# Kernel optimization log

Measured on AMD Instinct MI355X. Metric: run time of the kernel, lower is better.

Reference implementation:

```python
import jax, jax.numpy as jnp
import numpy as np

B, H, P, L = 8, 512, 512, 2048
HIGH_STAB, LOW_STAB = 0.9, 0.99  # 0 <= high < |lambda| <= low <= 1 (discrete dynamics)


def setup_inputs() -> dict:
    key = jax.random.key(0)
    k_u, k_mag, k_ph, k_b, k_c, k_d = jax.random.split(key, 6)
    u = jax.random.normal(k_u, (B, H, L), dtype=jnp.float32)
    # Frozen diagonal reservoir state matrix Lambda_bar: complex eigenvalues with
    # magnitude in (high_stability, low_stability], random phase (stored as real/imag pairs).
    mag = jax.random.uniform(k_mag, (P,), minval=HIGH_STAB, maxval=LOW_STAB)
    phase = jax.random.uniform(k_ph, (P,), minval=0.0, maxval=2.0 * np.pi)
    Lambda_bar_ri = jnp.stack([mag * jnp.cos(phase), mag * jnp.sin(phase)], axis=-1)  # (P,2)
    B_bar_ri = jax.random.normal(k_b, (P, H, 2), dtype=jnp.float32)  # complex B_bar as real pairs
    C_ri = jax.random.normal(k_c, (H, P, 2), dtype=jnp.float32)      # complex C as real pairs
    D = jax.random.normal(k_d, (H, H), dtype=jnp.float32)
    return {"u": u, "Lambda_bar_ri": Lambda_bar_ri, "B_bar_ri": B_bar_ri, "C_ri": C_ri, "D": D}


def _binary_op(e_i, e_j):
    A_i, Bu_i = e_i
    A_j, Bu_j = e_j
    return (A_j * A_i, A_j * Bu_i + Bu_j)


def reference(u, Lambda_bar_ri, B_bar_ri, C_ri, D):
    Lam = jax.lax.complex(Lambda_bar_ri[:, 0], Lambda_bar_ri[:, 1])        # (P,)
    B_bar = jax.lax.complex(B_bar_ri[..., 0], B_bar_ri[..., 1])            # (P,H)
    C = jax.lax.complex(C_ri[..., 0], C_ri[..., 1])                        # (H,P)
    # Bu_t = B_bar @ u_t for all t, batched: (B,P,L) complex
    Bu = jnp.einsum('ph,bhl->bpl', B_bar, u.astype(B_bar.dtype))
    A = jnp.broadcast_to(Lam[None, :, None], Bu.shape)                     # (B,P,L)
    # Parallel associative scan: x_t = Lam * x_{t-1} + Bu_t
    _, x = jax.lax.associative_scan(_binary_op, (A, Bu), axis=2)           # (B,P,L)
    C_A_Bu = jnp.einsum('hp,bpl->bhl', C, x).real                          # (B,H,L)
    # torch.einsum('hh,bhl->bhl', D, u) uses only the diagonal of D
    Du = jnp.diagonal(D)[None, :, None] * u
    return jax.nn.gelu(C_A_Bu + Du, approximate=False)
```

## Files before the change

kernel.cpp:

```cpp
#include <hip/hip_runtime.h>
#include <cstdint>
#include <cstddef>

#define BB 8
#define HH 512
#define PP 512
#define LL 2048

typedef __attribute__((ext_vector_type(8))) __bf16 bf16x8;
typedef __attribute__((ext_vector_type(4))) float f32x4;

__device__ __forceinline__ uint16_t f2bf(float f) {
  uint32_t u = __builtin_bit_cast(uint32_t, f);
  u += 0x7FFFu + ((u >> 16) & 1u);
  return (uint16_t)(u >> 16);
}

__device__ __forceinline__ void async_copy16(const void* gptr, void* ldsptr) {
  __builtin_amdgcn_global_load_lds(
      (const __attribute__((address_space(1))) unsigned int*)gptr,
      (__attribute__((address_space(3))) unsigned int*)ldsptr,
      16, 0, 0);
}

__global__ __launch_bounds__(256) void prep_and_transpose(
    const float* __restrict__ U, const float* __restrict__ Bbar,
    const float* __restrict__ Cri, const float* __restrict__ Dm,
    uint16_t* __restrict__ Ut, uint16_t* __restrict__ A1,
    uint16_t* __restrict__ A2, float* __restrict__ Dd) {
  __shared__ uint16_t tile[64][66];
  const int t = threadIdx.x;
  if (blockIdx.x < 2048) {
    const int bid = blockIdx.x;
    const int b = bid >> 8;
    const int h0 = ((bid >> 5) & 7) * 64;
    const int l0 = (bid & 31) * 64;
    const int r = t >> 2, c = t & 3;
    const float* src = U + ((size_t)(b * 512 + h0 + r)) * 2048 + l0 + c * 16;
#pragma unroll
    for (int q = 0; q < 4; ++q) {
      float4 v = *(const float4*)(src + q * 4);
      *(uint32_t*)&tile[r][c * 16 + q * 4]     = (uint32_t)f2bf(v.x) | ((uint32_t)f2bf(v.y) << 16);
      *(uint32_t*)&tile[r][c * 16 + q * 4 + 2] = (uint32_t)f2bf(v.z) | ((uint32_t)f2bf(v.w) << 16);
    }
    __syncthreads();
    uint16_t* dst = Ut + ((size_t)(b * 2048 + l0 + r)) * 512 + h0 + c * 16;
    uint32_t o[8];
#pragma unroll
    for (int k = 0; k < 8; ++k)
      o[k] = (uint32_t)tile[c * 16 + 2 * k][r] | ((uint32_t)tile[c * 16 + 2 * k + 1][r] << 16);
    *(uint4*)(dst)     = make_uint4(o[0], o[1], o[2], o[3]);
    *(uint4*)(dst + 8) = make_uint4(o[4], o[5], o[6], o[7]);
  } else {
    int idx = (blockIdx.x - 2048) * 256 + t;
    int p = idx >> 9, h = idx & 511;
    A1[(size_t)p * 512 + h]          = f2bf(Bbar[((size_t)p * 512 + h) * 2 + 0]);
    A1[(size_t)(512 + p) * 512 + h]  = f2bf(Bbar[((size_t)p * 512 + h) * 2 + 1]);
    int h2 = idx >> 9, p2 = idx & 511;
    A2[(size_t)h2 * 1024 + p2]        = f2bf( Cri[((size_t)h2 * 512 + p2) * 2 + 0]);
    A2[(size_t)h2 * 1024 + 512 + p2]  = f2bf(-Cri[((size_t)h2 * 512 + p2) * 2 + 1]);
    if (idx < 512) Dd[idx] = Dm[(size_t)idx * 512 + idx];
  }
}

__global__ __launch_bounds__(512) void scan_tr(
    const float* __restrict__ Lam, const uint16_t* __restrict__ Bu,
    uint16_t* __restrict__ Xt8) {
  __shared__ uint16_t S[16][2048];
  const int t = threadIdx.x, wave = t >> 6, lane = t & 63;
  const int b = blockIdx.x >> 6, p0 = (blockIdx.x & 63) * 8, p = p0 + wave;

  const float lr = Lam[p * 2 + 0], li = Lam[p * 2 + 1];
  float ar = lr, ai = li;
#pragma unroll
  for (int s = 0; s < 5; ++s) { float nr = ar * ar - ai * ai, ni = 2.f * ar * ai; ar = nr; ai = ni; }

  const uint16_t* rowre = Bu + ((size_t)(b * 1024 + p)) * 2048 + lane * 32;
  const uint16_t* rowim = Bu + ((size_t)(b * 1024 + 512 + p)) * 2048 + lane * 32;
  uint4 vr[4], vi[4];
#pragma unroll
  for (int q = 0; q < 4; ++q) { vr[q] = ((const uint4*)rowre)[q]; vi[q] = ((const uint4*)rowim)[q]; }

  float xr[32], xi[32];
  float sr = 0.f, si = 0.f;
#pragma unroll
  for (int q = 0; q < 4; ++q) {
    uint32_t wr[4] = {vr[q].x, vr[q].y, vr[q].z, vr[q].w};
    uint32_t wi[4] = {vi[q].x, vi[q].y, vi[q].z, vi[q].w};
#pragma unroll
    for (int d = 0; d < 4; ++d) {
      float br0 = __builtin_bit_cast(float, wr[d] << 16);
      float bi0 = __builtin_bit_cast(float, wi[d] << 16);
      float br1 = __builtin_bit_cast(float, wr[d] & 0xFFFF0000u);
      float bi1 = __builtin_bit_cast(float, wi[d] & 0xFFFF0000u);
      int j = q * 8 + d * 2;
      float nr = lr * sr - li * si + br0, ni = lr * si + li * sr + bi0;
      sr = nr; si = ni; xr[j] = sr; xi[j] = si;
      nr = lr * sr - li * si + br1; ni = lr * si + li * sr + bi1;
      sr = nr; si = ni; xr[j + 1] = sr; xi[j + 1] = si;
    }
  }
  float Ar = ar, Ai = ai, Sr = sr, Si = si;
#pragma unroll
  for (int off = 1; off < 64; off <<= 1) {
    float pAr = __shfl_up(Ar, off), pAi = __shfl_up(Ai, off);
    float pSr = __shfl_up(Sr, off), pSi = __shfl_up(Si, off);
    if (lane >= off) {
      float tSr = Ar * pSr - Ai * pSi + Sr;
      float tSi = Ar * pSi + Ai * pSr + Si;
      float tAr = Ar * pAr - Ai * pAi;
      float tAi = Ar * pAi + Ai * pAr;
      Sr = tSr; Si = tSi; Ar = tAr; Ai = tAi;
    }
  }
  float Cr = __shfl_up(Sr, 1), Ci = __shfl_up(Si, 1);
  if (lane == 0) { Cr = 0.f; Ci = 0.f; }
  float fr_ = lr * Cr - li * Ci, fi_ = lr * Ci + li * Cr;
#pragma unroll
  for (int j = 0; j < 32; ++j) {
    xr[j] += fr_; xi[j] += fi_;
    float nfr = fr_ * lr - fi_ * li, nfi = fr_ * li + fi_ * lr;
    fr_ = nfr; fi_ = nfi;
  }
#pragma unroll
  for (int q = 0; q < 4; ++q) {
    uint32_t wr[4], wi[4];
#pragma unroll
    for (int d = 0; d < 4; ++d) {
      int j = q * 8 + d * 2;
      wr[d] = (uint32_t)f2bf(xr[j]) | ((uint32_t)f2bf(xr[j + 1]) << 16);
      wi[d] = (uint32_t)f2bf(xi[j]) | ((uint32_t)f2bf(xi[j + 1]) << 16);
    }
    *(uint4*)&S[wave * 2 + 0][lane * 32 + q * 8] = make_uint4(wr[0], wr[1], wr[2], wr[3]);
    *(uint4*)&S[wave * 2 + 1][lane * 32 + q * 8] = make_uint4(wi[0], wi[1], wi[2], wi[3]);
  }
  __syncthreads();
  const size_t gre = (size_t)b * 128 + (p0 >> 3);
#pragma unroll
  for (int c = 0; c < 2; ++c) {
    uint16_t* dst = Xt8 + (gre + (size_t)c * 64) * 2048 * 8;
#pragma unroll
    for (int rep = 0; rep < 4; ++rep) {
      int l = rep * 512 + t;
      uint32_t o0 = (uint32_t)S[0 + c][l] | ((uint32_t)S[2 + c][l] << 16);
      uint32_t o1 = (uint32_t)S[4 + c][l] | ((uint32_t)S[6 + c][l] << 16);
      uint32_t o2 = (uint32_t)S[8 + c][l] | ((uint32_t)S[10 + c][l] << 16);
      uint32_t o3 = (uint32_t)S[12 + c][l] | ((uint32_t)S[14 + c][l] << 16);
      *(uint4*)(dst + (size_t)l * 8) = make_uint4(o0, o1, o2, o3);
    }
  }
}

#define GEMM_CORE(KDIM, PB0_EXPR, BSTRIDE)                                    \
  constexpr int K = (KDIM), NT = K / 32;                                      \
  __shared__ __align__(16) uint16_t Alds[3][128 * 32];                        \
  __shared__ __align__(16) uint16_t Blds[3][64 * 32];                         \
  const int t = threadIdx.x, lane = t & 63, w = t >> 6;                       \
  const int m0 = blockIdx.y * 128, n0 = blockIdx.x * 64, b = blockIdx.z;      \
  const int r0 = t >> 2;                                                      \
  const int c0 = (t & 3) ^ ((r0 >> 1) & 3);                                   \
  const uint16_t* pA0 = Amat + (size_t)(m0 + r0) * K + c0 * 8;                \
  const uint16_t* pA1 = Amat + (size_t)(m0 + 64 + r0) * K + c0 * 8;           \
  const uint16_t* pB0 = (PB0_EXPR);                                           \
  const int d0 = t * 8;                                                       \
  const int wm = (w >> 1) * 64, wn = (w & 1) * 32;                            \
  const int fr = lane & 15, fq = lane >> 4;                                   \
  int offA[4], offB[2];                                                       \
  _Pragma("unroll")                                                           \
  for (int i = 0; i < 4; ++i) {                                               \
    int rm = wm + i * 16 + fr;                                                \
    offA[i] = rm * 32 + ((fq ^ ((rm >> 1) & 3)) * 8);                         \
  }                                                                           \
  _Pragma("unroll")                                                           \
  for (int j = 0; j < 2; ++j) {                                               \
    int rn = wn + j * 16 + fr;                                                \
    offB[j] = rn * 32 + ((fq ^ ((rn >> 1) & 3)) * 8);                         \
  }                                                                           \
  f32x4 acc[4][2];                                                            \
  _Pragma("unroll")                                                           \
  for (int i = 0; i < 4; ++i)                                                 \
    _Pragma("unroll")                                                         \
    for (int j = 0; j < 2; ++j) acc[i][j] = (f32x4){0.f, 0.f, 0.f, 0.f};      \
            \
  async_copy16(pA0,             &Alds[0][d0]);                                \
  async_copy16(pA1,             &Alds[0][2048 + d0]);                         \
  async_copy16(pB0,             &Blds[0][d0]);                                \
  async_copy16(pA0 + 32,        &Alds[1][d0]);                                \
  async_copy16(pA1 + 32,        &Alds[1][2048 + d0]);                         \
  async_copy16(pB0 + (BSTRIDE), &Blds[1][d0]);                                \
  _Pragma("unroll")                                                           \
  for (int kt = 0; kt < NT; ++kt) {                                           \
    const int cur = kt % 3;                                                   \
    if (kt + 1 < NT) asm volatile("s_waitcnt vmcnt(3)" ::: "memory");         \
    else             asm volatile("s_waitcnt vmcnt(0)" ::: "memory");         \
    __builtin_amdgcn_s_barrier();                                             \
    __builtin_amdgcn_sched_barrier(0);                                        \
    if (kt + 2 < NT) {                                                        \
      const int nb = (kt + 2) % 3;                                            \
      const int kb = (kt + 2) * 32;                                           \
      async_copy16(pA0 + kb, &Alds[nb][d0]);                                  \
      async_copy16(pA1 + kb, &Alds[nb][2048 + d0]);                           \
      async_copy16(pB0 + (size_t)(kt + 2) * (BSTRIDE), &Blds[nb][d0]);        \
    }                                                                         \
    bf16x8 af[4], bv[2];                                                      \
    _Pragma("unroll")                                                         \
    for (int i = 0; i < 4; ++i) af[i] = *(const bf16x8*)&Alds[cur][offA[i]];  \
    _Pragma("unroll")                                                         \
    for (int j = 0; j < 2; ++j) bv[j] = *(const bf16x8*)&Blds[cur][offB[j]];  \
    _Pragma("unroll")                                                         \
    for (int i = 0; i < 4; ++i)                                               \
      _Pragma("unroll")                                                       \
      for (int j = 0; j < 2; ++j)                                             \
        acc[i][j] = __builtin_amdgcn_mfma_f32_16x16x32_bf16(af[i], bv[j], acc[i][j], 0, 0, 0); \
  }

__global__ __launch_bounds__(256) void gemm1_fused(
    const uint16_t* __restrict__ Amat, const uint16_t* __restrict__ Bt,
    uint16_t* __restrict__ Bu) {
  GEMM_CORE(512, Bt + ((size_t)b * 2048 + n0 + r0) * 512 + c0 * 8, 32)
  uint16_t* O = Bu + ((size_t)b * 1024 + m0) * 2048 + n0;
#pragma unroll
  for (int i = 0; i < 4; ++i)
#pragma unroll
    for (int j = 0; j < 2; ++j)
#pragma unroll
      for (int r = 0; r < 4; ++r) {
        int mm = wm + i * 16 + fq * 4 + r;
        int nn = wn + j * 16 + fr;
        O[(size_t)mm * 2048 + nn] = f2bf(acc[i][j][r]);
      }
}

__global__ __launch_bounds__(256) void gemm2_fused(
    const uint16_t* __restrict__ Amat, const uint16_t* __restrict__ Bt,
    float* __restrict__ Out, const float* __restrict__ Dd,
    const float* __restrict__ Uu) {
  GEMM_CORE(1024, Bt + (((size_t)b * 128 + c0) * 2048 + n0 + r0) * 8, 65536)
  const size_t base = ((size_t)b * 512 + m0) * 2048 + n0;
  float* O = Out + base;
  const float* Ub = Uu + base;
#pragma unroll
  for (int i = 0; i < 4; ++i)
#pragma unroll
    for (int r = 0; r < 4; ++r) {
      int mm = wm + i * 16 + fq * 4 + r;
      float dv = Dd[m0 + mm];
#pragma unroll
      for (int j = 0; j < 2; ++j) {
        int nn = wn + j * 16 + fr;
        float xv = acc[i][j][r] + dv * Ub[(size_t)mm * 2048 + nn];
        O[(size_t)mm * 2048 + nn] = 0.5f * xv * (1.f + erff(xv * 0.70710678118654752f));
      }
    }
}

extern "C" void kernel_launch(void* const* d_in, const int* in_sizes, int n_in,
                              void* d_out, int out_size, void* d_ws, size_t ws_size,
                              hipStream_t stream) {
  const float* u    = (const float*)d_in[0];
  const float* Lam  = (const float*)d_in[1];
  const float* Bbar = (const float*)d_in[2];
  const float* Cri  = (const float*)d_in[3];
  const float* Dm   = (const float*)d_in[4];
  float* out = (float*)d_out;

  char* ws = (char*)d_ws;
  uint16_t* Bu  = (uint16_t*)(ws);
  uint16_t* Xt8 = (uint16_t*)(ws + 33554432);
  uint16_t* Ut  = (uint16_t*)(ws + 33554432);
  uint16_t* A1 = (uint16_t*)(ws + 67108864);
  uint16_t* A2 = (uint16_t*)(ws + 68157440);
  float*    Dd = (float*)   (ws + 69206016);

  prep_and_transpose<<<3072, 256, 0, stream>>>(u, Bbar, Cri, Dm, Ut, A1, A2, Dd);
  gemm1_fused<<<dim3(32, 8, BB), 256, 0, stream>>>(A1, Ut, Bu);
  scan_tr<<<512, 512, 0, stream>>>(Lam, Bu, Xt8);
  gemm2_fused<<<dim3(32, 4, BB), 256, 0, stream>>>(A2, Xt8, out, Dd, u);
}
```

Before: 172.8 us.

## Swizzle scan LDS staging and switch GEMM to two-stage double buffering

```diff
diff --git a/kernel.cpp b/kernel.cpp
--- a/kernel.cpp
+++ b/kernel.cpp
@@ -122,6 +122,7 @@
     float nfr = fr_ * lr - fi_ * li, nfi = fr_ * li + fi_ * lr;
     fr_ = nfr; fi_ = nfi;
   }
+  const int wsw = (lane & 7) << 3;
 #pragma unroll
   for (int q = 0; q < 4; ++q) {
     uint32_t wr[4], wi[4];
@@ -131,8 +132,9 @@
       wr[d] = (uint32_t)f2bf(xr[j]) | ((uint32_t)f2bf(xr[j + 1]) << 16);
       wi[d] = (uint32_t)f2bf(xi[j]) | ((uint32_t)f2bf(xi[j + 1]) << 16);
     }
-    *(uint4*)&S[wave * 2 + 0][lane * 32 + q * 8] = make_uint4(wr[0], wr[1], wr[2], wr[3]);
-    *(uint4*)&S[wave * 2 + 1][lane * 32 + q * 8] = make_uint4(wi[0], wi[1], wi[2], wi[3]);
+    const int col = (lane * 32 + q * 8) ^ wsw;
+    *(uint4*)&S[wave * 2 + 0][col] = make_uint4(wr[0], wr[1], wr[2], wr[3]);
+    *(uint4*)&S[wave * 2 + 1][col] = make_uint4(wi[0], wi[1], wi[2], wi[3]);
   }
   __syncthreads();
   const size_t gre = (size_t)b * 128 + (p0 >> 3);
@@ -142,10 +144,11 @@
 #pragma unroll
     for (int rep = 0; rep < 4; ++rep) {
       int l = rep * 512 + t;
-      uint32_t o0 = (uint32_t)S[0 + c][l] | ((uint32_t)S[2 + c][l] << 16);
-      uint32_t o1 = (uint32_t)S[4 + c][l] | ((uint32_t)S[6 + c][l] << 16);
-      uint32_t o2 = (uint32_t)S[8 + c][l] | ((uint32_t)S[10 + c][l] << 16);
-      uint32_t o3 = (uint32_t)S[12 + c][l] | ((uint32_t)S[14 + c][l] << 16);
+      int ls = l ^ (((l >> 5) & 7) << 3);
+      uint32_t o0 = (uint32_t)S[0 + c][ls] | ((uint32_t)S[2 + c][ls] << 16);
+      uint32_t o1 = (uint32_t)S[4 + c][ls] | ((uint32_t)S[6 + c][ls] << 16);
+      uint32_t o2 = (uint32_t)S[8 + c][ls] | ((uint32_t)S[10 + c][ls] << 16);
+      uint32_t o3 = (uint32_t)S[12 + c][ls] | ((uint32_t)S[14 + c][ls] << 16);
       *(uint4*)(dst + (size_t)l * 8) = make_uint4(o0, o1, o2, o3);
     }
   }
@@ -153,8 +156,8 @@
 
 #define GEMM_CORE(KDIM, PB0_EXPR, BSTRIDE)                                    \
   constexpr int K = (KDIM), NT = K / 32;                                      \
-  __shared__ __align__(16) uint16_t Alds[3][128 * 32];                        \
-  __shared__ __align__(16) uint16_t Blds[3][64 * 32];                         \
+  __shared__ __align__(16) uint16_t Alds[2][128 * 32];                        \
+  __shared__ __align__(16) uint16_t Blds[2][64 * 32];                         \
   const int t = threadIdx.x, lane = t & 63, w = t >> 6;                       \
   const int m0 = blockIdx.y * 128, n0 = blockIdx.x * 64, b = blockIdx.z;      \
   const int r0 = t >> 2;                                                      \
@@ -181,26 +184,18 @@
   for (int i = 0; i < 4; ++i)                                                 \
     _Pragma("unroll")                                                         \
     for (int j = 0; j < 2; ++j) acc[i][j] = (f32x4){0.f, 0.f, 0.f, 0.f};      \
-            \
-  async_copy16(pA0,             &Alds[0][d0]);                                \
-  async_copy16(pA1,             &Alds[0][2048 + d0]);                         \
-  async_copy16(pB0,             &Blds[0][d0]);                                \
-  async_copy16(pA0 + 32,        &Alds[1][d0]);                                \
-  async_copy16(pA1 + 32,        &Alds[1][2048 + d0]);                         \
-  async_copy16(pB0 + (BSTRIDE), &Blds[1][d0]);                                \
-  _Pragma("unroll")                                                           \
-  for (int kt = 0; kt < NT; ++kt) {                                           \
-    const int cur = kt % 3;                                                   \
-    if (kt + 1 < NT) asm volatile("s_waitcnt vmcnt(3)" ::: "memory");         \
-    else             asm volatile("s_waitcnt vmcnt(0)" ::: "memory");         \
-    __builtin_amdgcn_s_barrier();                                             \
-    __builtin_amdgcn_sched_barrier(0);                                        \
-    if (kt + 2 < NT) {                                                        \
-      const int nb = (kt + 2) % 3;                                            \
-      const int kb = (kt + 2) * 32;                                           \
-      async_copy16(pA0 + kb, &Alds[nb][d0]);                                  \
-      async_copy16(pA1 + kb, &Alds[nb][2048 + d0]);                           \
-      async_copy16(pB0 + (size_t)(kt + 2) * (BSTRIDE), &Blds[nb][d0]);        \
+  async_copy16(pA0, &Alds[0][d0]);                                            \
+  async_copy16(pA1, &Alds[0][2048 + d0]);                                     \
+  async_copy16(pB0, &Blds[0][d0]);                                            \
+  __syncthreads();                                                            \
+  _Pragma("unroll 2")                                                         \
+  for (int it = 0; it < NT; ++it) {                                           \
+    const int cur = it & 1, nxt = cur ^ 1;                                    \
+    if (it + 1 < NT) {                                                        \
+      const int kb = (it + 1) * 32;                                           \
+      async_copy16(pA0 + kb, &Alds[nxt][d0]);                                 \
+      async_copy16(pA1 + kb, &Alds[nxt][2048 + d0]);                          \
+      async_copy16(pB0 + (size_t)(it + 1) * (BSTRIDE), &Blds[nxt][d0]);       \
     }                                                                         \
     bf16x8 af[4], bv[2];                                                      \
     _Pragma("unroll")                                                         \
@@ -212,6 +207,7 @@
       _Pragma("unroll")                                                       \
       for (int j = 0; j < 2; ++j)                                             \
         acc[i][j] = __builtin_amdgcn_mfma_f32_16x16x32_bf16(af[i], bv[j], acc[i][j], 0, 0, 0); \
+    __syncthreads();                                                          \
   }
 
 __global__ __launch_bounds__(256) void gemm1_fused(
```

Result: no change. 173.2 us (+0.2%).
